# Performance work log

Measured on AMD Instinct MI355X. Metric: run time of the kernel, lower is better.

## Reference

```python
import jax, jax.numpy as jnp
import numpy as np

NUM_TOKENS = 4096
LATENT_DIM = 256
BETA = 0.25
TEMPERATURE = 1.0  # temp_init buffer value
EPS_TEMP = 1e-6


def setup_inputs() -> dict:
    key = jax.random.key(0)
    k1, k2 = jax.random.split(key)
    latent = jax.random.normal(k1, (4, 2048, LATENT_DIM), dtype=jnp.float32)
    cb = jax.random.normal(k2, (NUM_TOKENS, LATENT_DIM), dtype=jnp.float32)
    # module normalizes codebook rows at init
    codebook = cb / jnp.linalg.norm(cb, axis=-1, keepdims=True)
    return {"latent": latent, "codebook": codebook}


def _l2norm(x):
    return x / jnp.clip(jnp.linalg.norm(x, axis=-1, keepdims=True), 1e-12)


def reference(latent, codebook):
    B, S, D = latent.shape
    flat = latent.reshape(-1, D)                       # [N, D]
    # cosine similarity via normalized matmul
    ln = _l2norm(flat)
    cn = _l2norm(codebook)
    cosine_sim = jnp.einsum('nd,kd->nk', ln, cn)       # [N, K]
    distances = 2.0 - 2.0 * cosine_sim
    scaled = distances / jnp.maximum(TEMPERATURE, EPS_TEMP)
    soft_assign = jax.nn.softmax(-scaled, axis=-1)     # [N, K]
    indices = jnp.argmax(soft_assign, axis=-1)         # [N]
    hard_assign = jax.nn.one_hot(indices, NUM_TOKENS, dtype=jnp.float32)
    # straight-through soft->hard assignment
    assign = hard_assign + soft_assign - jax.lax.stop_gradient(soft_assign)

    selected_cosine_sim = jnp.take_along_axis(cosine_sim, indices[:, None], axis=1).mean()

    # codebook pairwise euclidean diagnostics (off-diagonal mean / min)
    sq = jnp.sum(codebook * codebook, axis=-1)         # [K]
    d2 = sq[:, None] + sq[None, :] - 2.0 * (codebook @ codebook.T)
    cdist = jnp.sqrt(jnp.clip(d2, 0.0))                # [K, K]
    K = NUM_TOKENS
    off_sum = jnp.sum(cdist) - jnp.sum(jnp.diagonal(cdist))
    avg_euclidean = off_sum / (K * (K - 1))
    eye = jnp.eye(K, dtype=bool)
    min_euclidean = jnp.min(jnp.where(eye, jnp.inf, cdist))

    quantized = (assign @ codebook).reshape(B, S, D)
    commitment_loss = BETA * jnp.mean((jax.lax.stop_gradient(latent) - quantized) ** 2)
    codebook_loss = jnp.mean((latent - jax.lax.stop_gradient(quantized)) ** 2)
    quantized = latent + jax.lax.stop_gradient(quantized - latent)

    avg_probs = jnp.mean(hard_assign, axis=0)
    perplexity = jnp.exp(-jnp.sum(avg_probs * jnp.log(avg_probs + 1e-10)))

    return (quantized, indices, commitment_loss, codebook_loss, perplexity,
            selected_cosine_sim, avg_euclidean, min_euclidean)
```

## Files before the change

### kernel.cpp

```cpp
#include <hip/hip_runtime.h>
#include <hip/hip_bf16.h>
#include <math.h>

#define NTOK 8192
#define DIM 256
#define KCB 4096
#define NCB (KCB / 128)
#define NKEY 4
#define NKROW (NCB * NKEY)
#define DELTA 0.08f
#define GTIE 2e-6
#define MAXC 16
#define NPAIRB (NCB * (NCB + 1) / 2)
#define NSCOB (NCB * (NTOK / 128))

typedef unsigned long long ull;
typedef unsigned short ushort;
typedef __attribute__((ext_vector_type(8))) short shortx8;
typedef __attribute__((ext_vector_type(4))) float floatx4;
typedef const __attribute__((address_space(1))) void* gas_cp;
typedef __attribute__((address_space(3))) void* las_p;

__device__ __forceinline__ unsigned f2ord(float f) {
    unsigned u = __float_as_uint(f);
    return (u & 0x80000000u) ? ~u : (u | 0x80000000u);
}
__device__ __forceinline__ float ord2f(unsigned u) {
    unsigned b = (u & 0x80000000u) ? (u & 0x7FFFFFFFu) : ~u;
    return __uint_as_float(b);
}
__device__ __forceinline__ ushort f2bf(float f) {
    unsigned u = __float_as_uint(f);
    unsigned r = u + 0x7FFFu + ((u >> 16) & 1u);
    return (ushort)(r >> 16);
}

union TileSmem {
    struct { ushort a[128][64]; ushort b[128][64]; } t;
    unsigned keys[128][33];
    struct { float rs[128]; float rm[128]; } red;
};

__device__ __forceinline__ void stage_tile(const ushort* __restrict__ gbase,
                                           ushort (*lds)[64], int wave, int lane,
                                           int kk) {
    int p = lane & 7;
    int rsub = lane >> 3;
    int kc = p ^ (rsub & 7);
    const ushort* src0 = gbase + (size_t)(wave * 64 + rsub) * DIM + kk + kc * 8;
#pragma unroll
    for (int c = 0; c < 8; ++c) {
        const ushort* src = src0 + (size_t)(c * 8) * DIM;
        __builtin_amdgcn_global_load_lds((gas_cp)src, (las_p)&lds[wave * 64 + c * 8][0],
                                         16, 0, 0);
    }
}
__device__ __forceinline__ shortx8 frag_read(const ushort (*lds)[64], int row,
                                             int lc) {
    return *(const shortx8*)&lds[row][(lc ^ (row & 7)) * 8];
}

__device__ __forceinline__ float np_combine(const float* racc) {
    float h0 = __fadd_rn(__fadd_rn(__fadd_rn(racc[0], racc[1]), __fadd_rn(racc[2], racc[3])),
                         __fadd_rn(__fadd_rn(racc[4], racc[5]), __fadd_rn(racc[6], racc[7])));
    float h1 = __fadd_rn(__fadd_rn(__fadd_rn(racc[8], racc[9]), __fadd_rn(racc[10], racc[11])),
                         __fadd_rn(__fadd_rn(racc[12], racc[13]), __fadd_rn(racc[14], racc[15])));
    float s = __fadd_rn(h0, h1);
    return fmaxf(sqrtf(s), 1e-12f);
}

__global__ __launch_bounds__(256) void prep(const float* __restrict__ lat,
                                            const float* __restrict__ cb,
                                            float* __restrict__ nrml,
                                            float* __restrict__ nrmc,
                                            ushort* __restrict__ latbf,
                                            ushort* __restrict__ cnbf,
                                            ushort* __restrict__ cbbf,
                                            float* __restrict__ sq,
                                            unsigned* __restrict__ counts) {
    int bid = blockIdx.x, t = threadIdx.x;
    if (bid < NTOK) {
        int n = bid;
        if (n < KCB / 256) counts[n * 256 + t] = 0u;
        const float* row = lat + (size_t)n * DIM;
        latbf[(size_t)n * DIM + t] = f2bf(row[t]);
        __shared__ float racc[16];
        if (t < 16) {
            int h = t >> 3, j = t & 7;
            const float* p = row + h * 128;
            float r = __fmul_rn(p[j], p[j]);
#pragma unroll 1
            for (int i = 8; i < 128; i += 8)
                r = __fadd_rn(r, __fmul_rn(p[i + j], p[i + j]));
            racc[t] = r;
        }
        __syncthreads();
        if (t == 0) nrml[n] = np_combine(racc);
    } else {
        int n = bid - NTOK;
        __shared__ float racc2[16];
        __shared__ double dacc[16];
        __shared__ float snrm;
        const float* row = cb + (size_t)n * DIM;
        if (t < 16) {
            int h = t >> 3, j = t & 7;
            const float* p = row + h * 128;
            float r = __fmul_rn(p[j], p[j]);
            double ds = 0.0;
#pragma unroll 1
            for (int i = 8; i < 128; i += 8)
                r = __fadd_rn(r, __fmul_rn(p[i + j], p[i + j]));
#pragma unroll 1
            for (int i = 0; i < 128; i += 8) { double v = (double)p[i + j]; ds += v * v; }
            racc2[t] = r; dacc[t] = ds;
        }
        __syncthreads();
        if (t == 0) {
            float nr = np_combine(racc2);
            snrm = nr; nrmc[n] = nr;
            double ds = 0.0;
            for (int i = 0; i < 16; ++i) ds += dacc[i];
            sq[n] = (float)ds;
        }
        __syncthreads();
        float c = row[t];
        cnbf[(size_t)n * DIM + t] = f2bf(c / snrm);
        cbbf[(size_t)n * DIM + t] = f2bf(c);
    }
}

__global__ __launch_bounds__(128, 2) void gemms(const ushort* __restrict__ latbf,
                                                const ushort* __restrict__ cnbf,
                                                const ushort* __restrict__ cbbf,
                                                const float* __restrict__ sq,
                                                unsigned* __restrict__ keysw,
                                                float* __restrict__ psumw,
                                                unsigned* __restrict__ pminw) {
    __shared__ TileSmem sm;
    int tid = threadIdx.x;
    int wave = tid >> 6, lane = tid & 63;
    int quad = lane >> 4, l15 = lane & 15;
    int wrow = wave * 64;
    bool isScore = blockIdx.x < NSCOB;
    int rowBase, colBase, tri = 0;
    const ushort *gA, *gB;
    if (isScore) {
        int cbk = blockIdx.x & (NCB - 1);
        int rbk = blockIdx.x >> 5;
        rowBase = rbk * 128; colBase = cbk * 128;
        gA = latbf + (size_t)rowBase * DIM;
        gB = cnbf + (size_t)colBase * DIM;
    } else {
        tri = blockIdx.x - NSCOB;
        int a = (int)((sqrtf(8.f * tri + 1.f) - 1.f) * 0.5f);
        while ((a + 1) * (a + 2) / 2 <= tri) ++a;
        while (a * (a + 1) / 2 > tri) --a;
        int b = tri - a * (a + 1) / 2;
        rowBase = b * 128; colBase = a * 128;
        gA = cbbf + (size_t)rowBase * DIM;
        gB = cbbf + (size_t)colBase * DIM;
    }
    floatx4 acc[4][8];
#pragma unroll
    for (int m = 0; m < 4; ++m)
#pragma unroll
        for (int n = 0; n < 8; ++n) acc[m][n] = (floatx4){0.f, 0.f, 0.f, 0.f};
#pragma unroll 1
    for (int kk = 0; kk < DIM; kk += 64) {
        __syncthreads();
        stage_tile(gA, sm.t.a, wave, lane, kk);
        stage_tile(gB, sm.t.b, wave, lane, kk);
        __syncthreads();
#pragma unroll
        for (int s = 0; s < 2; ++s) {
            shortx8 af[4];
#pragma unroll
            for (int mt = 0; mt < 4; ++mt)
                af[mt] = frag_read(sm.t.a, wrow + mt * 16 + l15, s * 4 + quad);
#pragma unroll
            for (int nt = 0; nt < 8; ++nt) {
                shortx8 bfr = frag_read(sm.t.b, nt * 16 + l15, s * 4 + quad);
#pragma unroll
                for (int mt = 0; mt < 4; ++mt)
                    acc[mt][nt] = __builtin_amdgcn_mfma_f32_16x16x32_bf16(
                        af[mt], bfr, acc[mt][nt], 0, 0, 0);
            }
        }
    }
    __syncthreads();
    if (isScore) {
        unsigned colp[8];
#pragma unroll
        for (int nt = 0; nt < 8; ++nt)
            colp[nt] = 4095u - (unsigned)(colBase + nt * 16 + l15);
#pragma unroll
        for (int mt = 0; mt < 4; ++mt)
#pragma unroll
            for (int reg = 0; reg < 4; ++reg) {
                unsigned b1 = 0u, b2 = 0u;
#pragma unroll
                for (int nt = 0; nt < 8; ++nt) {
                    unsigned key = (f2ord(acc[mt][nt][reg]) & 0xFFFFF000u) | colp[nt];
                    unsigned lo = min(key, b1);
                    b1 = max(key, b1);
                    b2 = max(lo, b2);
                }
                int row = wrow + mt * 16 + quad * 4 + reg;
                uint2 kv; kv.x = b1; kv.y = b2;
                *(uint2*)&sm.keys[row][l15 * 2] = kv;
            }
        __syncthreads();
        {
            unsigned a0 = 0, a1 = 0, a2 = 0, a3 = 0;
#pragma unroll
            for (int j = 0; j < 8; ++j) {
                uint4 v4 = *(const uint4*)&sm.keys[tid][j * 4];
                unsigned vs[4] = {v4.x, v4.y, v4.z, v4.w};
#pragma unroll
                for (int q = 0; q < 4; ++q) {
                    unsigned v = vs[q];
                    unsigned n0 = min(v, a0); a0 = max(v, a0);
                    unsigned n1 = min(n0, a1); a1 = max(n0, a1);
                    unsigned n2 = min(n1, a2); a2 = max(n1, a2);
                    a3 = max(n2, a3);
                }
            }
            size_t base = (size_t)(rowBase + tid) * NKROW + (blockIdx.x & (NCB - 1)) * NKEY;
            uint4 o; o.x = a0; o.y = a1; o.z = a2; o.w = a3;
            *(uint4*)&keysw[base] = o;
        }
    } else {
        float lsum = 0.f, lmin = INFINITY;
#pragma unroll
        for (int mt = 0; mt < 4; ++mt)
#pragma unroll
            for (int reg = 0; reg < 4; ++reg) {
                int i = rowBase + wrow + mt * 16 + quad * 4 + reg;
                float sqi = sq[i];
#pragma unroll
                for (int nt = 0; nt < 8; ++nt) {
                    int j = colBase + nt * 16 + l15;
                    float d2 = sqi + sq[j] - 2.0f * acc[mt][nt][reg];
                    float d = sqrtf(fmaxf(d2, 0.0f));
                    bool use = i < j;
                    lsum += use ? d : 0.f;
                    lmin = fminf(lmin, use ? d : INFINITY);
                }
            }
        sm.red.rs[tid] = lsum; sm.red.rm[tid] = lmin; __syncthreads();
        for (int s = 64; s > 0; s >>= 1) {
            if (tid < s) {
                sm.red.rs[tid] += sm.red.rs[tid + s];
                sm.red.rm[tid] = fminf(sm.red.rm[tid], sm.red.rm[tid + s]);
            }
            __syncthreads();
        }
        if (tid == 0) { psumw[tri] = sm.red.rs[0]; pminw[tri] = f2ord(sm.red.rm[0]); }
    }
}

__global__ __launch_bounds__(256) void argmax_resolve(const float* __restrict__ lat,
                                                      const float* __restrict__ cb,
                                                      const float* __restrict__ nrml,
                                                      const float* __restrict__ nrmc,
                                                      const unsigned* __restrict__ keysw,
                                                      float* __restrict__ outidx,
                                                      float* __restrict__ outq,
                                                      unsigned* __restrict__ counts,
                                                      float* __restrict__ selw,
                                                      float* __restrict__ msew) {
    __shared__ int scand[4][MAXC];
    __shared__ double sc64[4][MAXC];
    int wid = threadIdx.x >> 6, lane = threadIdx.x & 63;
    int n = blockIdx.x * 4 + wid;
    const unsigned* kr = keysw + (size_t)n * NKROW;
    uint2 kv = *(const uint2*)(kr + lane * 2);
    unsigned m = max(kv.x, kv.y);
#pragma unroll
    for (int off = 1; off < 64; off <<= 1) {
        unsigned o = __shfl_xor(m, off, 64);
        m = max(m, o);
    }
    float v1 = ord2f(m & 0xFFFFF000u);
    float thresh = v1 - DELTA;
    bool p0 = ord2f(kv.x & 0xFFFFF000u) >= thresh;
    bool p1 = ord2f(kv.y & 0xFFFFF000u) >= thresh;
    ull b0 = __ballot(p0), b1 = __ballot(p1);
    int below0 = __builtin_amdgcn_mbcnt_hi((unsigned)(b0 >> 32),
                 __builtin_amdgcn_mbcnt_lo((unsigned)b0, 0));
    int below1 = __builtin_amdgcn_mbcnt_hi((unsigned)(b1 >> 32),
                 __builtin_amdgcn_mbcnt_lo((unsigned)b1, 0));
    int base1 = __popcll(b0);
    int nc = base1 + __popcll(b1);
    if (p0 && below0 < MAXC)
        scand[wid][below0] = 4095 - (int)(kv.x & 0xFFFu);
    if (p1 && base1 + below1 < MAXC)
        scand[wid][base1 + below1] = 4095 - (int)(kv.y & 0xFFFu);
    nc = nc < MAXC ? nc : MAXC;
    __threadfence_block();
    float nx = nrml[n];
    int d0 = lane * 4;
    float4 xv = *(const float4*)(lat + (size_t)n * DIM + d0);
    int idx; float selcos;
    if (nc <= 1) {
        idx = 4095 - (int)(m & 0xFFFu);
        selcos = v1 / nx;
    } else {
        float la0 = xv.x / nx, la1 = xv.y / nx, la2 = xv.z / nx, la3 = xv.w / nx;
        for (int c = 0; c < nc; ++c) {
            int k = scand[wid][c];
            float nk = nrmc[k];
            float4 cv = *(const float4*)(cb + (size_t)k * DIM + d0);
            double part = (double)(cv.x / nk) * la0 + (double)(cv.y / nk) * la1 +
                          (double)(cv.z / nk) * la2 + (double)(cv.w / nk) * la3;
#pragma unroll
            for (int off = 1; off < 64; off <<= 1) part += __shfl_xor(part, off, 64);
            if (lane == 0) sc64[wid][c] = part;
        }
        __threadfence_block();
        double best64 = -1e300;
        for (int c = 0; c < nc; ++c) best64 = fmax(best64, sc64[wid][c]);
        int nrisk = 0;
        for (int c = 0; c < nc; ++c) if (sc64[wid][c] >= best64 - GTIE) ++nrisk;
        if (nrisk == 1) {
            idx = 0x7FFFFFFF; selcos = 0.f;
            for (int c = 0; c < nc; ++c)
                if (sc64[wid][c] >= best64 - GTIE) { idx = scand[wid][c]; selcos = (float)sc64[wid][c]; }
        } else {
            ull keyf = 0ull, keym = 0ull;
            if (lane < nc && sc64[wid][lane] >= best64 - GTIE) {
                int k = scand[wid][lane];
                const float* cr = cb + (size_t)k * DIM;
                const float* x = lat + (size_t)n * DIM;
                float nk = nrmc[k];
                float af = 0.f, am = 0.f;
                for (int d = 0; d < DIM; ++d) {
                    float la = x[d] / nx;
                    float cv = cr[d] / nk;
                    af = fmaf(la, cv, af);
                    am = __fadd_rn(am, __fmul_rn(la, cv));
                }
                float df = __fsub_rn(2.0f, __fmul_rn(2.0f, af));
                float dm = __fsub_rn(2.0f, __fmul_rn(2.0f, am));
                keyf = ((ull)(0xFFFFFFFFu - f2ord(df)) << 32) | (ull)(0xFFFFFFFFu - (unsigned)k);
                keym = ((ull)(0xFFFFFFFFu - f2ord(dm)) << 32) | (ull)(0xFFFFFFFFu - (unsigned)k);
            }
#pragma unroll
            for (int off = 1; off < 64; off <<= 1) {
                ull of = __shfl_xor(keyf, off, 64);
                ull om = __shfl_xor(keym, off, 64);
                keyf = of > keyf ? of : keyf;
                keym = om > keym ? om : keym;
            }
            int colf = (int)(0xFFFFFFFFu - (unsigned)(keyf & 0xFFFFFFFFull));
            int colm = (int)(0xFFFFFFFFu - (unsigned)(keym & 0xFFFFFFFFull));
            idx = colf < colm ? colf : colm;
            selcos = 0.f;
            for (int c = 0; c < nc; ++c)
                if (scand[wid][c] == idx) selcos = (float)sc64[wid][c];
        }
    }
    float4 qv = *(const float4*)(cb + (size_t)idx * DIM + d0);
    *(float4*)(outq + (size_t)n * DIM + d0) = qv;
    float dx = xv.x - qv.x, dy = xv.y - qv.y, dz = xv.z - qv.z, dw = xv.w - qv.w;
    float msep = fmaf(dx, dx, fmaf(dy, dy, fmaf(dz, dz, dw * dw)));
#pragma unroll
    for (int off = 1; off < 64; off <<= 1) msep += __shfl_xor(msep, off, 64);
    if (lane == 0) {
        outidx[n] = (float)idx;
        atomicAdd(&counts[idx], 1u);
        selw[n] = selcos;
        msew[n] = msep;
    }
}

__global__ void finalize(const unsigned* __restrict__ counts,
                         const float* __restrict__ selw,
                         const float* __restrict__ msew,
                         const float* __restrict__ psumw,
                         const unsigned* __restrict__ pminw,
                         float* __restrict__ outs) {
    int t = threadIdx.x;
    __shared__ float red[256];
    float h = 0.f;
    for (int k = t; k < KCB; k += 256) {
        float p = (float)counts[k] * (1.0f / (float)NTOK);
        h += p * logf(p + 1e-10f);
    }
    red[t] = h; __syncthreads();
    for (int s = 128; s > 0; s >>= 1) { if (t < s) red[t] += red[t + s]; __syncthreads(); }
    float entNeg = red[0];
    __syncthreads();
    float ssel = 0.f;
    for (int k = t; k < NTOK; k += 256) ssel += selw[k];
    red[t] = ssel; __syncthreads();
    for (int s = 128; s > 0; s >>= 1) { if (t < s) red[t] += red[t + s]; __syncthreads(); }
    float selSum = red[0];
    __syncthreads();
    float sm = 0.f;
    for (int k = t; k < NTOK; k += 256) sm += msew[k];
    red[t] = sm; __syncthreads();
    for (int s = 128; s > 0; s >>= 1) { if (t < s) red[t] += red[t + s]; __syncthreads(); }
    float mseSum = red[0];
    __syncthreads();
    float ps = 0.f;
    for (int k = t; k < NPAIRB; k += 256) ps += psumw[k];
    red[t] = ps; __syncthreads();
    for (int s = 128; s > 0; s >>= 1) { if (t < s) red[t] += red[t + s]; __syncthreads(); }
    float pairSum = red[0];
    __syncthreads();
    unsigned pm = 0xFFFFFFFFu;
    for (int k = t; k < NPAIRB; k += 256) pm = min(pm, pminw[k]);
    ((unsigned*)red)[t] = pm; __syncthreads();
    for (int s = 128; s > 0; s >>= 1) {
        if (t < s) ((unsigned*)red)[t] = min(((unsigned*)red)[t], ((unsigned*)red)[t + s]);
        __syncthreads();
    }
    unsigned pairMin = ((unsigned*)red)[0];
    if (t == 0) {
        float mse = mseSum / (float)(NTOK * DIM);
        outs[0] = 0.25f * mse;
        outs[1] = mse;
        outs[2] = expf(-entNeg);
        outs[3] = selSum / (float)NTOK;
        outs[4] = pairSum * 2.0f / ((float)KCB * (float)(KCB - 1));
        outs[5] = ord2f(pairMin);
    }
}

extern "C" void kernel_launch(void* const* d_in, const int* in_sizes, int n_in,
                              void* d_out, int out_size, void* d_ws, size_t ws_size,
                              hipStream_t stream) {
    const float* latent = (const float*)d_in[0];
    const float* codebook = (const float*)d_in[1];
    float* out = (float*)d_out;
    float* outq = out;
    float* outidx = out + (size_t)NTOK * DIM;
    float* outs = outidx + NTOK;

    unsigned* keysw = (unsigned*)d_ws;
    ushort* latbf = (ushort*)(keysw + (size_t)NKROW * NTOK);
    ushort* cnbf = latbf + (size_t)NTOK * DIM;
    ushort* cbbf = cnbf + (size_t)KCB * DIM;
    float* nrml = (float*)(cbbf + (size_t)KCB * DIM);
    float* nrmc = nrml + NTOK;
    float* sq = nrmc + KCB;
    unsigned* counts = (unsigned*)(sq + KCB);
    float* selw = (float*)(counts + KCB);
    float* msew = selw + NTOK;
    float* psumw = msew + NTOK;
    unsigned* pminw = (unsigned*)(psumw + NPAIRB);

    hipLaunchKernelGGL(prep, dim3(NTOK + KCB), dim3(256), 0, stream,
                       latent, codebook, nrml, nrmc, latbf, cnbf, cbbf, sq, counts);
    hipLaunchKernelGGL(gemms, dim3(NSCOB + NPAIRB), dim3(128), 0, stream,
                       latbf, cnbf, cbbf, sq, keysw, psumw, pminw);
    hipLaunchKernelGGL(argmax_resolve, dim3(NTOK / 4), dim3(256), 0, stream,
                       latent, codebook, nrml, nrmc, keysw, outidx, outq, counts, selw, msew);
    hipLaunchKernelGGL(finalize, dim3(1), dim3(256), 0, stream, counts, selw, msew, psumw, pminw, outs);
}
```

Baseline: 176.2 us.

## Enlarge GEMM block tile to 256x128 with four waves

Doubles the row dimension of each GEMM block tile, from 128 to 256, and uses 256 threads (4 waves) per block for both the score and codebook-pair GEMMs. The triangular pair enumeration is remapped to 256x128 tiles. The aim is to cut the number of blocks and the redundant global/LDS loads of B tiles by reusing each B tile across more rows. The cost is more LDS per block and the loss of the 2-blocks-per-CU launch bound, which may lower occupancy. The hidden epilogue code must also handle the new tile shape and pair mapping correctly.

```diff
diff --git a/kernel.cpp b/kernel.cpp
--- a/kernel.cpp
+++ b/kernel.cpp
@@ -11,8 +11,8 @@
 #define DELTA 0.08f
 #define GTIE 2e-6
 #define MAXC 16
-#define NPAIRB (NCB * (NCB + 1) / 2)
-#define NSCOB (NCB * (NTOK / 128))
+#define NSCOB ((NTOK / 256) * NCB)
+#define NPAIRB 272
 
 typedef unsigned long long ull;
 typedef unsigned short ushort;
@@ -36,14 +36,14 @@
 }
 
 union TileSmem {
-    struct { ushort a[128][64]; ushort b[128][64]; } t;
-    unsigned keys[128][33];
-    struct { float rs[128]; float rm[128]; } red;
+    struct { ushort a[256][64]; ushort b[128][64]; } t;
+    unsigned keys[256][33];
+    struct { float rs[256]; float rm[256]; } red;
 };
 
-__device__ __forceinline__ void stage_tile(const ushort* __restrict__ gbase,
-                                           ushort (*lds)[64], int wave, int lane,
-                                           int kk) {
+__device__ __forceinline__ void stage_rows64(const ushort* __restrict__ gbase,
+                                             ushort (*lds)[64], int wave, int lane,
+                                             int kk) {
     int p = lane & 7;
     int rsub = lane >> 3;
     int kc = p ^ (rsub & 7);
@@ -52,6 +52,20 @@
     for (int c = 0; c < 8; ++c) {
         const ushort* src = src0 + (size_t)(c * 8) * DIM;
         __builtin_amdgcn_global_load_lds((gas_cp)src, (las_p)&lds[wave * 64 + c * 8][0],
+                                         16, 0, 0);
+    }
+}
+__device__ __forceinline__ void stage_rows32(const ushort* __restrict__ gbase,
+                                             ushort (*lds)[64], int wave, int lane,
+                                             int kk) {
+    int p = lane & 7;
+    int rsub = lane >> 3;
+    int kc = p ^ (rsub & 7);
+    const ushort* src0 = gbase + (size_t)(wave * 32 + rsub) * DIM + kk + kc * 8;
+#pragma unroll
+    for (int c = 0; c < 4; ++c) {
+        const ushort* src = src0 + (size_t)(c * 8) * DIM;
+        __builtin_amdgcn_global_load_lds((gas_cp)src, (las_p)&lds[wave * 32 + c * 8][0],
                                          16, 0, 0);
     }
 }
@@ -129,13 +143,13 @@
     }
 }
 
-__global__ __launch_bounds__(128, 2) void gemms(const ushort* __restrict__ latbf,
-                                                const ushort* __restrict__ cnbf,
-                                                const ushort* __restrict__ cbbf,
-                                                const float* __restrict__ sq,
-                                                unsigned* __restrict__ keysw,
-                                                float* __restrict__ psumw,
-                                                unsigned* __restrict__ pminw) {
+__global__ __launch_bounds__(256) void gemms(const ushort* __restrict__ latbf,
+                                             const ushort* __restrict__ cnbf,
+                                             const ushort* __restrict__ cbbf,
+                                             const float* __restrict__ sq,
+                                             unsigned* __restrict__ keysw,
+                                             float* __restrict__ psumw,
+                                             unsigned* __restrict__ pminw) {
     __shared__ TileSmem sm;
     int tid = threadIdx.x;
     int wave = tid >> 6, lane = tid & 63;
@@ -147,16 +161,15 @@
     if (isScore) {
         int cbk = blockIdx.x & (NCB - 1);
         int rbk = blockIdx.x >> 5;
-        rowBase = rbk * 128; colBase = cbk * 128;
+        rowBase = rbk * 256; colBase = cbk * 128;
         gA = latbf + (size_t)rowBase * DIM;
         gB = cnbf + (size_t)colBase * DIM;
     } else {
         tri = blockIdx.x - NSCOB;
-        int a = (int)((sqrtf(8.f * tri + 1.f) - 1.f) * 0.5f);
-        while ((a + 1) * (a + 2) / 2 <= tri) ++a;
-        while (a * (a + 1) / 2 > tri) --a;
-        int b = tri - a * (a + 1) / 2;
-        rowBase = b * 128; colBase = a * 128;
+        int rb = 0;
+        while ((rb + 1) * (33 - (rb + 1)) <= tri) ++rb;
+        int cbk = tri - rb * (33 - rb) + 2 * rb;
+        rowBase = rb * 256; colBase = cbk * 128;
         gA = cbbf + (size_t)rowBase * DIM;
         gB = cbbf + (size_t)colBase * DIM;
     }
@@ -168,8 +181,8 @@
 #pragma unroll 1
     for (int kk = 0; kk < DIM; kk += 64) {
         __syncthreads();
-        stage_tile(gA, sm.t.a, wave, lane, kk);
-        stage_tile(gB, sm.t.b, wave, lane, kk);
+        stage_rows64(gA, sm.t.a, wave, lane, kk);
+        stage_rows32(gB, sm.t.b, wave, lane, kk);
         __syncthreads();
 #pragma unroll
         for (int s = 0; s < 2; ++s) {
@@ -248,7 +261,7 @@
                 }
             }
         sm.red.rs[tid] = lsum; sm.red.rm[tid] = lmin; __syncthreads();
-        for (int s = 64; s > 0; s >>= 1) {
+        for (int s = 128; s > 0; s >>= 1) {
             if (tid < s) {
                 sm.red.rs[tid] += sm.red.rs[tid + s];
                 sm.red.rm[tid] = fminf(sm.red.rm[tid], sm.red.rm[tid + s]);
@@ -453,7 +466,7 @@
 
     hipLaunchKernelGGL(prep, dim3(NTOK + KCB), dim3(256), 0, stream,
                        latent, codebook, nrml, nrmc, latbf, cnbf, cbbf, sq, counts);
-    hipLaunchKernelGGL(gemms, dim3(NSCOB + NPAIRB), dim3(128), 0, stream,
+    hipLaunchKernelGGL(gemms, dim3(NSCOB + NPAIRB), dim3(256), 0, stream,
                        latbf, cnbf, cbbf, sq, keysw, psumw, pminw);
     hipLaunchKernelGGL(argmax_resolve, dim3(NTOK / 4), dim3(256), 0, stream,
                        latent, codebook, nrml, nrmc, keysw, outidx, outq, counts, selw, msew);
```

Result: slower. 205.7 us (+16.8%).
